# Optimization experiments

Measured on AMD Instinct MI355X. Metric: run time of the kernel, lower is better.

Reference implementation:

```python
import jax, jax.numpy as jnp
import numpy as np

B = 8192          # batch_size
NB = 4096         # num_banks (== mask length)
PAD = NB // 2     # reflect pad on each side


def setup_inputs() -> dict:
    key = jax.random.key(0)
    k1, k2, k3 = jax.random.split(key, 3)
    logits = jax.random.normal(k1, (NB,), dtype=jnp.float32) * 0.1
    u = jax.random.uniform(k2, (B, NB), dtype=jnp.float32)          # Bernoulli uniforms
    shift = jax.random.randint(k3, (B,), 0, NB, dtype=jnp.int32)    # per-sample shift
    return {"logits": logits, "u": u, "shift": shift}


def reference(logits, u, shift):
    # Bernoulli(sigmoid(logits)) sample via inverse-CDF on externally supplied uniforms
    p = jax.nn.sigmoid(logits)                       # (NB,)
    grid = (u < p).astype(jnp.float32)               # (B, NB)
    # Bernoulli log_prob summed over banks: g*log(p) + (1-g)*log(1-p)
    log_probs = (grid * jax.nn.log_sigmoid(logits)
                 + (1.0 - grid) * jax.nn.log_sigmoid(-logits)).sum(axis=1)  # (B,)
    # reflect-pad along bank axis, then gather a shifted window of length NB
    padded = jnp.pad(grid, ((0, 0), (PAD, PAD)), mode="reflect")    # (B, NB+2*PAD)
    idx = shift[:, None].astype(jnp.int32) + jnp.arange(NB, dtype=jnp.int32)[None, :]
    masks = jnp.take_along_axis(padded, idx, axis=1)[:, None, :]    # (B, 1, NB)
    return masks, log_probs
```

## Files before the change

kernel.cpp:

```cpp
#include <hip/hip_runtime.h>
#include <math.h>

#define NB 4096
#define PAD 2048
#define BLOCK 256
#define ITERS (NB / 4 / BLOCK)

__device__ __forceinline__ int mirror_idx(int i) {
    i = ::abs(i);
    return (i < NB) ? i : (2 * (NB - 1) - i);
}

__global__ void fbmp_precompute(const float* __restrict__ logits, float* __restrict__ ws) {
    int j = blockIdx.x * blockDim.x + threadIdx.x;
    if (j >= NB) return;
    float x = logits[j];
    double xd = (double)x;
    float e = (float)exp(-xd);
    float p = 1.0f / (1.0f + e);
    float lsp = (float)(-log1p(exp(-xd)));
    float lsn = (float)(-log1p(exp(xd)));
    ws[j] = p;
    ws[NB + j] = lsp;
    ws[2 * NB + j] = lsn;
}

__global__ __launch_bounds__(BLOCK, 8) void fbmp_main(
    const float* __restrict__ u, const int* __restrict__ shift,
    const float* __restrict__ ws,
    float* __restrict__ masks, float* __restrict__ logp)
{
    __shared__ float sg[NB];
    __shared__ float sred[BLOCK / 64];

    const int b = blockIdx.x;
    const int s = shift[b] - PAD;

    const float4* __restrict__ u4   = (const float4*)(u + (size_t)b * NB);
    const float4* __restrict__ p4   = (const float4*)(ws);
    const float4* __restrict__ lsp4 = (const float4*)(ws + NB);
    const float4* __restrict__ lsn4 = (const float4*)(ws + 2 * NB);

    float acc = 0.0f;
    {
        const int t = threadIdx.x;
        float4 uv = u4[t];
        float4 pv = p4[t];
        float4 ap = lsp4[t];
        float4 an = lsn4[t];
        #pragma unroll
        for (int it = 0; it < ITERS; ++it) {
            float4 nuv, npv, nap, nan2;
            if (it + 1 < ITERS) {
                const int i1 = t + (it + 1) * BLOCK;
                nuv = u4[i1];
                npv = p4[i1];
                nap = lsp4[i1];
                nan2 = lsn4[i1];
            }
            const int i = t + it * BLOCK;
            bool c0 = uv.x < pv.x;
            bool c1 = uv.y < pv.y;
            bool c2 = uv.z < pv.z;
            bool c3 = uv.w < pv.w;
            acc += (c0 ? ap.x : an.x) + (c1 ? ap.y : an.y)
                 + (c2 ? ap.z : an.z) + (c3 ? ap.w : an.w);
            float4 g;
            g.x = c0 ? 1.0f : 0.0f;
            g.y = c1 ? 1.0f : 0.0f;
            g.z = c2 ? 1.0f : 0.0f;
            g.w = c3 ? 1.0f : 0.0f;
            ((float4*)sg)[i] = g;
            uv = nuv; pv = npv; ap = nap; an = nan2;
        }
    }

    #pragma unroll
    for (int off = 32; off > 0; off >>= 1)
        acc += __shfl_down(acc, off, 64);
    const int lane = threadIdx.x & 63;
    const int wid  = threadIdx.x >> 6;
    if (lane == 0) sred[wid] = acc;
    __syncthreads();
    if (threadIdx.x == 0) {
        float t = 0.0f;
        #pragma unroll
        for (int w = 0; w < BLOCK / 64; ++w) t += sred[w];
        logp[b] = t;
    }

    float* __restrict__ mrow = masks + (size_t)b * NB;
    #pragma unroll
    for (int it = 0; it < NB / BLOCK; ++it) {
        const int k = threadIdx.x + it * BLOCK;
        float v = sg[mirror_idx(k + s)];
        __builtin_nontemporal_store(v, &mrow[k]);
    }
}

extern "C" void kernel_launch(void* const* d_in, const int* in_sizes, int n_in,
                              void* d_out, int out_size, void* d_ws, size_t ws_size,
                              hipStream_t stream) {
    const float* logits = (const float*)d_in[0];
    const float* u      = (const float*)d_in[1];
    const int*   shift  = (const int*)d_in[2];
    const int B = in_sizes[2];

    float* ws    = (float*)d_ws;
    float* masks = (float*)d_out;
    float* logp  = (float*)d_out + (size_t)B * NB;

    fbmp_precompute<<<(NB + 255) / 256, 256, 0, stream>>>(logits, ws);
    fbmp_main<<<B, BLOCK, 0, stream>>>(u, shift, ws, masks, logp);
}
```

Baseline: 240.7 us.

## Process eight rows per block with register-cached tables and double-buffered LDS

Each block now handles eight batch rows. The p/log-sigmoid tables are loaded into registers once per block instead of once per row, the next row's uniforms are prefetched while the current row's mask is written, and a two-slot shared buffer is used so only one barrier is needed per row. Mask stores are widened to 4-float nontemporal vector stores. The cost is fewer blocks (1024), higher register pressure with occupancy hint lowered to 4, and scalar LDS gathers to build each vector.

```diff
diff --git a/kernel.cpp b/kernel.cpp
--- a/kernel.cpp
+++ b/kernel.cpp
@@ -4,7 +4,10 @@
 #define NB 4096
 #define PAD 2048
 #define BLOCK 256
-#define ITERS (NB / 4 / BLOCK)
+#define ROWS 8
+#define QITERS (NB / 4 / BLOCK)
+
+typedef float f32x4 __attribute__((ext_vector_type(4)));
 
 __device__ __forceinline__ int mirror_idx(int i) {
     i = ::abs(i);
@@ -25,76 +28,97 @@
     ws[2 * NB + j] = lsn;
 }
 
-__global__ __launch_bounds__(BLOCK, 8) void fbmp_main(
+__global__ __launch_bounds__(BLOCK, 4) void fbmp_main(
     const float* __restrict__ u, const int* __restrict__ shift,
     const float* __restrict__ ws,
-    float* __restrict__ masks, float* __restrict__ logp)
+    float* __restrict__ masks, float* __restrict__ logp, int B)
 {
-    __shared__ float sg[NB];
-    __shared__ float sred[BLOCK / 64];
+    __shared__ float sg[2][NB];
+    __shared__ float sred[2][BLOCK / 64];
 
-    const int b = blockIdx.x;
-    const int s = shift[b] - PAD;
+    const int t  = threadIdx.x;
+    const int b0 = blockIdx.x * ROWS;
+    const int nrows = (B - b0 < ROWS) ? (B - b0) : ROWS;
 
-    const float4* __restrict__ u4   = (const float4*)(u + (size_t)b * NB);
     const float4* __restrict__ p4   = (const float4*)(ws);
     const float4* __restrict__ lsp4 = (const float4*)(ws + NB);
     const float4* __restrict__ lsn4 = (const float4*)(ws + 2 * NB);
 
-    float acc = 0.0f;
+    float4 pv[QITERS], ap[QITERS], an[QITERS];
+    #pragma unroll
+    for (int it = 0; it < QITERS; ++it) {
+        pv[it] = p4[t + it * BLOCK];
+        ap[it] = lsp4[t + it * BLOCK];
+        an[it] = lsn4[t + it * BLOCK];
+    }
+
+    float4 uv[QITERS];
     {
-        const int t = threadIdx.x;
-        float4 uv = u4[t];
-        float4 pv = p4[t];
-        float4 ap = lsp4[t];
-        float4 an = lsn4[t];
+        const float4* __restrict__ u4 = (const float4*)(u + (size_t)b0 * NB);
         #pragma unroll
-        for (int it = 0; it < ITERS; ++it) {
-            float4 nuv, npv, nap, nan2;
-            if (it + 1 < ITERS) {
-                const int i1 = t + (it + 1) * BLOCK;
-                nuv = u4[i1];
-                npv = p4[i1];
-                nap = lsp4[i1];
-                nan2 = lsn4[i1];
-            }
-            const int i = t + it * BLOCK;
-            bool c0 = uv.x < pv.x;
-            bool c1 = uv.y < pv.y;
-            bool c2 = uv.z < pv.z;
-            bool c3 = uv.w < pv.w;
-            acc += (c0 ? ap.x : an.x) + (c1 ? ap.y : an.y)
-                 + (c2 ? ap.z : an.z) + (c3 ? ap.w : an.w);
+        for (int it = 0; it < QITERS; ++it) uv[it] = u4[t + it * BLOCK];
+    }
+    int s_cur = shift[b0] - PAD;
+
+    const int lane = t & 63;
+    const int wid  = t >> 6;
+
+    for (int r = 0; r < nrows; ++r) {
+        const int buf = r & 1;
+
+        float acc = 0.0f;
+        #pragma unroll
+        for (int it = 0; it < QITERS; ++it) {
+            bool c0 = uv[it].x < pv[it].x;
+            bool c1 = uv[it].y < pv[it].y;
+            bool c2 = uv[it].z < pv[it].z;
+            bool c3 = uv[it].w < pv[it].w;
+            acc += (c0 ? ap[it].x : an[it].x) + (c1 ? ap[it].y : an[it].y)
+                 + (c2 ? ap[it].z : an[it].z) + (c3 ? ap[it].w : an[it].w);
             float4 g;
             g.x = c0 ? 1.0f : 0.0f;
             g.y = c1 ? 1.0f : 0.0f;
             g.z = c2 ? 1.0f : 0.0f;
             g.w = c3 ? 1.0f : 0.0f;
-            ((float4*)sg)[i] = g;
-            uv = nuv; pv = npv; ap = nap; an = nan2;
+            ((float4*)sg[buf])[t + it * BLOCK] = g;
         }
-    }
 
-    #pragma unroll
-    for (int off = 32; off > 0; off >>= 1)
-        acc += __shfl_down(acc, off, 64);
-    const int lane = threadIdx.x & 63;
-    const int wid  = threadIdx.x >> 6;
-    if (lane == 0) sred[wid] = acc;
-    __syncthreads();
-    if (threadIdx.x == 0) {
-        float t = 0.0f;
         #pragma unroll
-        for (int w = 0; w < BLOCK / 64; ++w) t += sred[w];
-        logp[b] = t;
-    }
+        for (int off = 32; off > 0; off >>= 1)
+            acc += __shfl_down(acc, off, 64);
+        if (lane == 0) sred[buf][wid] = acc;
 
-    float* __restrict__ mrow = masks + (size_t)b * NB;
-    #pragma unroll
-    for (int it = 0; it < NB / BLOCK; ++it) {
-        const int k = threadIdx.x + it * BLOCK;
-        float v = sg[mirror_idx(k + s)];
-        __builtin_nontemporal_store(v, &mrow[k]);
+        int s_next = 0;
+        if (r + 1 < nrows) {
+            const float4* __restrict__ un4 =
+                (const float4*)(u + (size_t)(b0 + r + 1) * NB);
+            #pragma unroll
+            for (int it = 0; it < QITERS; ++it) uv[it] = un4[t + it * BLOCK];
+            s_next = shift[b0 + r + 1] - PAD;
+        }
+
+        __syncthreads();
+
+        float* __restrict__ mrow = masks + (size_t)(b0 + r) * NB;
+        const float* __restrict__ sgb = sg[buf];
+        #pragma unroll
+        for (int it = 0; it < QITERS; ++it) {
+            const int i = t + it * BLOCK;
+            const int k = 4 * i + s_cur;
+            f32x4 o;
+            o.x = sgb[mirror_idx(k + 0)];
+            o.y = sgb[mirror_idx(k + 1)];
+            o.z = sgb[mirror_idx(k + 2)];
+            o.w = sgb[mirror_idx(k + 3)];
+            __builtin_nontemporal_store(o, (f32x4*)mrow + i);
+        }
+        if (t == 0) {
+            float tt = 0.0f;
+            #pragma unroll
+            for (int w = 0; w < BLOCK / 64; ++w) tt += sred[buf][w];
+            logp[b0 + r] = tt;
+        }
+        s_cur = s_next;
     }
 }
 
@@ -111,5 +135,6 @@
     float* logp  = (float*)d_out + (size_t)B * NB;
 
     fbmp_precompute<<<(NB + 255) / 256, 256, 0, stream>>>(logits, ws);
-    fbmp_main<<<B, BLOCK, 0, stream>>>(u, shift, ws, masks, logp);
+    const int grid = (B + ROWS - 1) / ROWS;
+    fbmp_main<<<grid, BLOCK, 0, stream>>>(u, shift, ws, masks, logp, B);
 }
```

After: 246.9 us. +2.6%, slower.
